# Kernel tuning notes

Hardware: AMD Instinct MI355X
Metric: run time of the kernel (lower is better)

Reference implementation:

```python
import jax, jax.numpy as jnp
import numpy as np

NUM_FIELDS = 39
_ROW, _COL = np.triu_indices(NUM_FIELDS, k=1)  # 741 pairs, matches the double loop in __init__


def setup_inputs() -> dict:
    key = jax.random.key(0)
    x = jax.random.normal(key, (16384, NUM_FIELDS, 64), dtype=jnp.float32)
    return {"x": x}


def reference(x) -> jnp.ndarray:
    # Original: p=x[:,row,:,None], q=x[:,col,None,:], pq=p@q (B,P,d,d), then sum over both d axes.
    # sum_{a,b} p_a * q_b == (sum_a p_a) * (sum_b q_b), so we fuse and never build the d x d outer.
    s = jnp.sum(x, axis=-1)                     # [B, F] per-field embedding sums
    return s[:, _ROW] * s[:, _COL]              # [B, P] with P = F*(F-1)/2 = 741
```

## Files before the change

### kernel.cpp

```cpp
#include <hip/hip_runtime.h>

#define NF 39
#define NP 741
#define N4 624

struct PairLUT { unsigned short rc[NP]; };

constexpr PairLUT make_lut() {
    PairLUT L{};
    int p = 0;
    for (int i = 0; i < NF; ++i)
        for (int j = i + 1; j < NF; ++j) {
            L.rc[p] = (unsigned short)((i << 8) | j);
            ++p;
        }
    return L;
}

__constant__ PairLUT LUT = make_lut();

__global__ __launch_bounds__(256) void opn_kernel(const float* __restrict__ x,
                                                  float* __restrict__ out) {
    const int tid = threadIdx.x;
    const int wid = tid >> 6;
    const int l   = tid & 63;
    const int b   = blockIdx.x * 4 + wid;

    __shared__ float s[4][NF + 1];

    const float4* xb4 = reinterpret_cast<const float4*>(x) + (size_t)b * N4;

    float v[10];
    #pragma unroll
    for (int r = 0; r < 9; ++r) {
        const float4 t = xb4[r * 64 + l];
        v[r] = (t.x + t.y) + (t.z + t.w);
    }
    {
        float4 t = {0.f, 0.f, 0.f, 0.f};
        if (576 + l < N4) t = xb4[576 + l];
        v[9] = (t.x + t.y) + (t.z + t.w);
    }

    #pragma unroll
    for (int r = 0; r < 10; ++r) {
        float vv = v[r];
        vv += __shfl_xor(vv, 1);
        vv += __shfl_xor(vv, 2);
        vv += __shfl_xor(vv, 4);
        vv += __shfl_xor(vv, 8);
        const int f = r * 4 + (l >> 4);
        if ((l & 15) == 0 && f < NF) s[wid][f] = vv;
    }

    float* ob = out + (size_t)b * NP;
    #pragma unroll
    for (int k = 0; k < 12; ++k) {
        const int p = k * 64 + l;
        if (p < NP) {
            const unsigned int rc = LUT.rc[p];
            __builtin_nontemporal_store(s[wid][rc >> 8] * s[wid][rc & 255u], ob + p);
        }
    }
}

extern "C" void kernel_launch(void* const* d_in, const int* in_sizes, int n_in,
                              void* d_out, int out_size, void* d_ws, size_t ws_size,
                              hipStream_t stream) {
    const float* x = (const float*)d_in[0];
    float* out = (float*)d_out;
    const int B = in_sizes[0] / (NF * 64);
    opn_kernel<<<B / 4, 256, 0, stream>>>(x, out);
}
```

Measured before the change: 37.28 us.

## Process four rows per wave with double-buffered register prefetch

Each wavefront now handles four batch rows instead of one, loading the next row's float4 data into registers while the current row is reduced and its pair products stored. The grid shrinks by four accordingly. This aims to keep more loads in flight per wave and amortise per-block overhead, at the cost of higher register pressure and fewer blocks, which could reduce occupancy and latency hiding.

```diff
diff --git a/kernel.cpp b/kernel.cpp
--- a/kernel.cpp
+++ b/kernel.cpp
@@ -19,49 +19,62 @@
 
 __constant__ PairLUT LUT = make_lut();
 
+__device__ __forceinline__ void load_row(const float4* __restrict__ xb4, int l,
+                                         float4 (&t)[10]) {
+    #pragma unroll
+    for (int r = 0; r < 9; ++r) t[r] = xb4[r * 64 + l];
+    t[9] = make_float4(0.f, 0.f, 0.f, 0.f);
+    if (l < 48) t[9] = xb4[576 + l];
+}
+
+__device__ __forceinline__ void process_row(const float4 (&t)[10], int l,
+                                            float* __restrict__ srow,
+                                            float* __restrict__ ob) {
+    #pragma unroll
+    for (int r = 0; r < 10; ++r) {
+        float vv = (t[r].x + t[r].y) + (t[r].z + t[r].w);
+        vv += __shfl_xor(vv, 1);
+        vv += __shfl_xor(vv, 2);
+        vv += __shfl_xor(vv, 4);
+        vv += __shfl_xor(vv, 8);
+        const int f = r * 4 + (l >> 4);
+        if ((l & 15) == 0 && f < NF) srow[f] = vv;
+    }
+    #pragma unroll
+    for (int k = 0; k < 12; ++k) {
+        const int p = k * 64 + l;
+        if (p < NP) {
+            const unsigned int rc = LUT.rc[p];
+            __builtin_nontemporal_store(srow[rc >> 8] * srow[rc & 255u], ob + p);
+        }
+    }
+}
+
 __global__ __launch_bounds__(256) void opn_kernel(const float* __restrict__ x,
                                                   float* __restrict__ out) {
     const int tid = threadIdx.x;
     const int wid = tid >> 6;
     const int l   = tid & 63;
-    const int b   = blockIdx.x * 4 + wid;
+    const int gw  = blockIdx.x * 4 + wid;
+    const size_t b0 = (size_t)gw * 4;
 
     __shared__ float s[4][NF + 1];
+    float* srow = s[wid];
 
-    const float4* xb4 = reinterpret_cast<const float4*>(x) + (size_t)b * N4;
+    const float4* x4 = reinterpret_cast<const float4*>(x);
 
-    float v[10];
-    #pragma unroll
-    for (int r = 0; r < 9; ++r) {
-        const float4 t = xb4[r * 64 + l];
-        v[r] = (t.x + t.y) + (t.z + t.w);
-    }
-    {
-        float4 t = {0.f, 0.f, 0.f, 0.f};
-        if (576 + l < N4) t = xb4[576 + l];
-        v[9] = (t.x + t.y) + (t.z + t.w);
-    }
+    float4 ta[10], tb[10];
+    load_row(x4 + b0 * N4,       l, ta);
+    load_row(x4 + (b0 + 1) * N4, l, tb);
 
-    #pragma unroll
-    for (int r = 0; r < 10; ++r) {
-        float vv = v[r];
-        vv += __shfl_xor(vv, 1);
-        vv += __shfl_xor(vv, 2);
-        vv += __shfl_xor(vv, 4);
-        vv += __shfl_xor(vv, 8);
-        const int f = r * 4 + (l >> 4);
-        if ((l & 15) == 0 && f < NF) s[wid][f] = vv;
-    }
+    process_row(ta, l, srow, out + b0 * NP);
+    load_row(x4 + (b0 + 2) * N4, l, ta);
 
-    float* ob = out + (size_t)b * NP;
-    #pragma unroll
-    for (int k = 0; k < 12; ++k) {
-        const int p = k * 64 + l;
-        if (p < NP) {
-            const unsigned int rc = LUT.rc[p];
-            __builtin_nontemporal_store(s[wid][rc >> 8] * s[wid][rc & 255u], ob + p);
-        }
-    }
+    process_row(tb, l, srow, out + (b0 + 1) * NP);
+    load_row(x4 + (b0 + 3) * N4, l, tb);
+
+    process_row(ta, l, srow, out + (b0 + 2) * NP);
+    process_row(tb, l, srow, out + (b0 + 3) * NP);
 }
 
 extern "C" void kernel_launch(void* const* d_in, const int* in_sizes, int n_in,
@@ -70,5 +83,5 @@
     const float* x = (const float*)d_in[0];
     float* out = (float*)d_out;
     const int B = in_sizes[0] / (NF * 64);
-    opn_kernel<<<B / 4, 256, 0, stream>>>(x, out);
+    opn_kernel<<<B / 16, 256, 0, stream>>>(x, out);
 }
```

Result: slower. 39.01 us (+4.6%).
